# Optimization experiments

Hardware: AMD Instinct MI355X
Metric: run time of the kernel (lower is better)

## Reference

```python
import jax, jax.numpy as jnp
import numpy as np

D_MODEL = 1024
N_HEADS = 16
D_HEAD = D_MODEL // N_HEADS
BATCH = 2
SEQ = 2048


def spectral_linear(x, basis, scales):
    # (x @ U) * s @ U^T ; basis is a fixed (non-learned) square matrix
    return ((x @ basis) * scales) @ basis.T


def setup_inputs() -> dict:
    key = jax.random.key(0)
    ks = jax.random.split(key, 3)
    x = jax.random.normal(ks[0], (BATCH, SEQ, D_MODEL), dtype=jnp.float32)
    # orthonormal-ish spectral basis (random Gaussian scaled keeps values sane)
    basis = jax.random.normal(ks[1], (D_MODEL, D_MODEL), dtype=jnp.float32) / np.sqrt(D_MODEL)
    route_bias = jax.random.normal(ks[2], (N_HEADS, SEQ, SEQ), dtype=jnp.float32) * 0.02
    ones = jnp.ones((D_MODEL,), dtype=jnp.float32)
    return {
        "x": x,
        "basis": basis,
        "scale_q": ones,
        "scale_k": ones,
        "scale_v": ones,
        "scale_o": ones,
        "route_bias": route_bias,
    }


def reference(x, basis, scale_q, scale_k, scale_v, scale_o, route_bias):
    bsz, seq_len, _ = x.shape

    def split_heads(t):  # [b,s,d] -> [b,h,s,dh]
        return t.reshape(bsz, seq_len, N_HEADS, D_HEAD).transpose(0, 2, 1, 3)

    q = split_heads(spectral_linear(x, basis, scale_q))
    k = split_heads(spectral_linear(x, basis, scale_k))
    v = split_heads(spectral_linear(x, basis, scale_v))

    scores = jnp.einsum("bhqd,bhkd->bhqk", q, k) / np.sqrt(D_HEAD).astype(np.float32)
    scores = scores + route_bias[None, :, :seq_len, :seq_len]
    causal = jnp.triu(jnp.ones((seq_len, seq_len), dtype=bool), k=1)
    scores = jnp.where(causal[None, None], -jnp.inf, scores)
    attn = jax.nn.softmax(scores, axis=-1)
    out = jnp.einsum("bhqk,bhkd->bhqd", attn, v)
    out = out.transpose(0, 2, 1, 3).reshape(bsz, seq_len, D_MODEL)
    return spectral_linear(out, basis, scale_o)
```

## Files before the change

kernel.cpp:

```cpp
#include <hip/hip_runtime.h>
#include <stdint.h>

#define AS1 __attribute__((address_space(1)))
#define AS3 __attribute__((address_space(3)))

typedef __bf16 bf16x8 __attribute__((ext_vector_type(8)));
typedef float f32x4 __attribute__((ext_vector_type(4)));

#if defined(__has_builtin)
#if __has_builtin(__builtin_amdgcn_global_load_lds)
#define USE_GLL 1
#else
#define USE_GLL 0
#endif
#else
#define USE_GLL 0
#endif

static __device__ __forceinline__ unsigned short f2bf(float f) {
    union { float f; uint32_t u; } v; v.f = f;
    uint32_t u = v.u + 0x7fffu + ((v.u >> 16) & 1u);
    return (unsigned short)(u >> 16);
}

__global__ void k_prep(const float* __restrict__ x, const float* __restrict__ basis,
                       const float* __restrict__ sq, const float* __restrict__ sk,
                       const float* __restrict__ sv, const float* __restrict__ so,
                       unsigned short* __restrict__ x_bf,
                       unsigned short* __restrict__ Bq, unsigned short* __restrict__ Bk,
                       unsigned short* __restrict__ Bv, unsigned short* __restrict__ Bo,
                       unsigned short* __restrict__ Ub) {
    int b = blockIdx.x;
    if (b < 4096) {
        int idx = b * 256 + threadIdx.x;
        int k = idx & 1023;
        float v = basis[idx];
        Bq[idx] = f2bf(v * sq[k]);
        Bk[idx] = f2bf(v * sk[k]);
        Bv[idx] = f2bf(v * sv[k]);
        Bo[idx] = f2bf(v * so[k]);
        Ub[idx] = f2bf(v);
    } else {
        int idx = ((b - 4096) * 256 + threadIdx.x) * 4;
        float4 v = *(const float4*)(x + idx);
        unsigned short r[4] = { f2bf(v.x), f2bf(v.y), f2bf(v.z), f2bf(v.w) };
        *(uint2*)(x_bf + idx) = *(const uint2*)r;
    }
}

__global__ void k_transpose_v(const unsigned short* __restrict__ vsb, unsigned short* __restrict__ vtb) {
    __shared__ __align__(16) unsigned short t[128 * 72];
    const int sc = blockIdx.x;
    const int bh = blockIdx.y;
    const int tid = threadIdx.x;
    #pragma unroll
    for (int rep = 0; rep < 4; ++rep) {
        int idx = rep * 256 + tid;
        int s = idx >> 3, part = idx & 7;
        *(uint4*)(t + s * 72 + part * 8) =
            *(const uint4*)(vsb + ((size_t)bh * 2048 + sc * 128 + s) * 64 + part * 8);
    }
    __syncthreads();
    #pragma unroll
    for (int rep = 0; rep < 4; ++rep) {
        int idx = rep * 256 + tid;
        int d = idx >> 4, pc = idx & 15;
        unsigned short tmp[8];
        #pragma unroll
        for (int j = 0; j < 8; ++j) tmp[j] = t[(pc * 8 + j) * 72 + d];
        *(uint4*)(vtb + ((size_t)bh * 64 + d) * 2048 + sc * 128 + pc * 8) = *(const uint4*)tmp;
    }
}

__global__ __launch_bounds__(512, 2)
void k_gemm_qkv8(const unsigned short* __restrict__ A,
                 const unsigned short* __restrict__ B,
                 unsigned short* __restrict__ qkv)
{
    __shared__ __align__(16) unsigned short lds[3 * 16384];

    const int tid  = threadIdx.x;
    const int lane = tid & 63;
    const int w    = tid >> 6;
    const int wm   = w & 1;
    const int wn   = w >> 1;
    const int fm   = lane & 15;
    const int quad = lane >> 4;
    const int K    = 1024;
    const int NT   = 32;

    int bid  = blockIdx.y * 12 + blockIdx.x;
    int sbid = (bid & 7) * 24 + (bid >> 3);
    const int bm = sbid / 12;
    const int bn = sbid % 12;

    const int srow = tid >> 2;
    const int sg   = tid & 3;
    const unsigned short* gA = A + ((size_t)(bm * 256) + srow) * K + sg * 8;
    const unsigned short* gB = B + ((size_t)(bn * 256) + srow) * K + sg * 8;

#define STAGE_A8(tt, h) __builtin_amdgcn_global_load_lds( \
        (const void AS1*)(gA + (size_t)(h) * 128 * 1024 + (tt) * 32), \
        (void AS3*)(lds + ((tt) % 3) * 16384 + (h) * 4096 + w * 512), 16, 0, 0)
#define STAGE_B8(tt, h) __builtin_amdgcn_global_load_lds( \
        (const void AS1*)(gB + (size_t)(h) * 128 * 1024 + (tt) * 32), \
        (void AS3*)(lds + ((tt) % 3) * 16384 + 8192 + (h) * 4096 + w * 512), 16, 0, 0)

    f32x4 zero4 = {0.f, 0.f, 0.f, 0.f};
    f32x4 acc[8][4];
    #pragma unroll
    for (int i = 0; i < 8; ++i)
        #pragma unroll
        for (int j = 0; j < 4; ++j) acc[i][j] = zero4;

    STAGE_A8(0, 0); STAGE_A8(0, 1); STAGE_B8(0, 0); STAGE_B8(0, 1);
    STAGE_A8(1, 0); STAGE_A8(1, 1); STAGE_B8(1, 0); STAGE_B8(1, 1);
    asm volatile("s_waitcnt vmcnt(4)" ::: "memory");
    __builtin_amdgcn_s_barrier();

    for (int t = 0; t < NT; ++t) {
        const unsigned short* buf = lds + (t % 3) * 16384;

        bf16x8 bfr[4], af[4];
        #pragma unroll
        for (int j = 0; j < 4; ++j)
            bfr[j] = *(const bf16x8*)(buf + 8192 + (wn * 64 + j * 16 + fm) * 32 + quad * 8);
        #pragma unroll
        for (int i = 0; i < 4; ++i)
            af[i] = *(const bf16x8*)(buf + (wm * 128 + i * 16 + fm) * 32 + quad * 8);
        if (t + 2 < NT) { STAGE_A8(t + 2, 0); STAGE_A8(t + 2, 1); }
        __builtin_amdgcn_s_barrier();
        asm volatile("s_waitcnt lgkmcnt(0)" ::: "memory");
        __builtin_amdgcn_s_setprio(1);
        #pragma unroll
        for (int i = 0; i < 4; ++i)
            #pragma unroll
            for (int j = 0; j < 4; ++j)
                acc[i][j] = __builtin_amdgcn_mfma_f32_16x16x32_bf16(af[i], bfr[j], acc[i][j], 0, 0, 0);
        __builtin_amdgcn_s_setprio(0);
        __builtin_amdgcn_s_barrier();

        bf16x8 af2[4];
        #pragma unroll
        for (int i = 0; i < 4; ++i)
            af2[i] = *(const bf16x8*)(buf + (wm * 128 + 64 + i * 16 + fm) * 32 + quad * 8);
        if (t + 2 < NT) { STAGE_B8(t + 2, 0); STAGE_B8(t + 2, 1); }
        if (t < NT - 2)       asm volatile("s_waitcnt vmcnt(4)" ::: "memory");
        else if (t == NT - 2) asm volatile("s_waitcnt vmcnt(0)" ::: "memory");
        __builtin_amdgcn_s_barrier();
        asm volatile("s_waitcnt lgkmcnt(0)" ::: "memory");
        __builtin_amdgcn_s_setprio(1);
        #pragma unroll
        for (int i = 0; i < 4; ++i)
            #pragma unroll
            for (int j = 0; j < 4; ++j)
                acc[i + 4][j] = __builtin_amdgcn_mfma_f32_16x16x32_bf16(af2[i], bfr[j], acc[i + 4][j], 0, 0, 0);
        __builtin_amdgcn_s_setprio(0);
        __builtin_amdgcn_s_barrier();
    }
#undef STAGE_A8
#undef STAGE_B8

    #pragma unroll
    for (int i = 0; i < 8; ++i)
        #pragma unroll
        for (int j = 0; j < 4; ++j)
            #pragma unroll
            for (int r = 0; r < 4; ++r) {
                int row = bm * 256 + wm * 128 + i * 16 + quad * 4 + r;
                int col = bn * 256 + wn * 64 + j * 16 + fm;
                int sec = col >> 10, cc = col & 1023;
                int bb = row >> 11, s = row & 2047;
                int hh = cc >> 6,  d = cc & 63;
                qkv[((size_t)sec << 22) + (((size_t)(bb * 16 + hh)) * 2048 + s) * 64 + d] = f2bf(acc[i][j][r]);
            }
}

#define BK 32
template<int EPI>
__global__ __launch_bounds__(256, 2)
void k_gemm_n64(const unsigned short* __restrict__ A,
                const unsigned short* __restrict__ B,
                void* __restrict__ Cout,
                int M, int N, int K)
{
    __shared__ __align__(16) unsigned short As[128 * BK];
    __shared__ __align__(16) unsigned short Bs[64 * BK];

    const int tid  = threadIdx.x;
    const int lane = tid & 63;
    const int w    = tid >> 6;
    const int wm   = w & 1;
    const int wn   = w >> 1;
    const int bm   = blockIdx.y;
    const int bn   = blockIdx.x;
    const int fm   = lane & 15;
    const int quad = lane >> 4;
    const int fk   = quad * 8;
    const int srow = lane >> 2;
    const int spart= lane & 3;

    f32x4 zero4 = {0.f, 0.f, 0.f, 0.f};
    f32x4 acc[4][2];
    #pragma unroll
    for (int i = 0; i < 4; ++i)
        #pragma unroll
        for (int j = 0; j < 2; ++j) acc[i][j] = zero4;

    for (int k0 = 0; k0 < K; k0 += BK) {
        #pragma unroll
        for (int t = 0; t < 2; ++t) {
            int row = w * 32 + t * 16 + srow;
            const unsigned short* ga = A + (size_t)(bm * 128 + row) * K + k0 + spart * 8;
#if USE_GLL
            __builtin_amdgcn_global_load_lds((const void AS1*)ga, (void AS3*)(As + w * 1024 + t * 512), 16, 0, 0);
#else
            *(uint4*)(As + w * 1024 + t * 512 + lane * 8) = *(const uint4*)ga;
#endif
        }
        {
            const unsigned short* gb = B + (size_t)(bn * 64 + w * 16 + srow) * K + k0 + spart * 8;
#if USE_GLL
            __builtin_amdgcn_global_load_lds((const void AS1*)gb, (void AS3*)(Bs + w * 512), 16, 0, 0);
#else
            *(uint4*)(Bs + w * 512 + lane * 8) = *(const uint4*)gb;
#endif
        }
        __syncthreads();
        bf16x8 af[4], bfr[2];
        #pragma unroll
        for (int i = 0; i < 4; ++i) af[i] = *(const bf16x8*)(As + (wm * 64 + i * 16 + fm) * BK + fk);
        #pragma unroll
        for (int j = 0; j < 2; ++j) bfr[j] = *(const bf16x8*)(Bs + (wn * 32 + j * 16 + fm) * BK + fk);
        #pragma unroll
        for (int i = 0; i < 4; ++i)
            #pragma unroll
            for (int j = 0; j < 2; ++j)
                acc[i][j] = __builtin_amdgcn_mfma_f32_16x16x32_bf16(af[i], bfr[j], acc[i][j], 0, 0, 0);
        __syncthreads();
    }

    #pragma unroll
    for (int i = 0; i < 4; ++i)
        #pragma unroll
        for (int j = 0; j < 2; ++j)
            #pragma unroll
            for (int r = 0; r < 4; ++r) {
                int row = bm * 128 + wm * 64 + i * 16 + quad * 4 + r;
                int col = bn * 64 + wn * 32 + j * 16 + fm;
                if (EPI == 0) ((unsigned short*)Cout)[(size_t)row * N + col] = f2bf(acc[i][j][r]);
                else          ((float*)Cout)[(size_t)row * N + col] = acc[i][j][r];
            }
}

__global__ __launch_bounds__(256, 2)
void k_attn(const unsigned short* __restrict__ qs, const unsigned short* __restrict__ ks,
            const unsigned short* __restrict__ vt, const float* __restrict__ bias,
            unsigned short* __restrict__ out)
{
    const int qt = 15 - blockIdx.x;
    const int by = blockIdx.y;
    const int h  = by >> 1;
    const int b  = by & 1;
    const int bh = b * 16 + h;
    const size_t rowbase = (size_t)bh * 2048;

    const int tid  = threadIdx.x;
    const int lane = tid & 63;
    const int w    = tid >> 6;
    const int fm   = lane & 15;
    const int quad = lane >> 4;
    const int fk   = quad * 8;

    __shared__ __align__(16) unsigned short Ks[64 * 72];
    __shared__ __align__(16) unsigned short Vt[64 * 72];
    __shared__ __align__(16) unsigned short Ps[4][32 * 72];

    const int q0 = qt * 128 + w * 32;

    bf16x8 qf[2][2];
    #pragma unroll
    for (int g = 0; g < 2; ++g)
        #pragma unroll
        for (int c = 0; c < 2; ++c)
            qf[g][c] = *(const bf16x8*)(qs + (rowbase + q0 + g * 16 + fm) * 64 + c * 32 + fk);

    f32x4 zero4 = {0.f, 0.f, 0.f, 0.f};
    f32x4 oacc[2][4];
    float lsum[2][4];
    #pragma unroll
    for (int g = 0; g < 2; ++g) {
        #pragma unroll
        for (int jd = 0; jd < 4; ++jd) oacc[g][jd] = zero4;
        #pragma unroll
        for (int r = 0; r < 4; ++r) lsum[g][r] = 0.f;
    }

    const int nkt = qt * 2 + 2;
    for (int kt = 0; kt < nkt; ++kt) {
        float bb[2][4][4];
        #pragma unroll
        for (int g = 0; g < 2; ++g)
            #pragma unroll
            for (int jn = 0; jn < 4; ++jn)
                #pragma unroll
                for (int r = 0; r < 4; ++r)
                    bb[g][jn][r] = bias[((size_t)h * 2048 + q0 + g * 16 + quad * 4 + r) * 2048
                                        + kt * 64 + jn * 16 + fm];

        #pragma unroll
        for (int rep = 0; rep < 2; ++rep) {
            int idx  = rep * 256 + tid;
            int row  = idx >> 3;
            int part = idx & 7;
            *(uint4*)(Ks + row * 72 + part * 8) =
                *(const uint4*)(ks + (rowbase + kt * 64 + row) * 64 + part * 8);
            *(uint4*)(Vt + row * 72 + part * 8) =
                *(const uint4*)(vt + ((size_t)bh * 64 + row) * 2048 + kt * 64 + part * 8);
        }
        __syncthreads();

        bf16x8 kb[4][2];
        #pragma unroll
        for (int jn = 0; jn < 4; ++jn)
            #pragma unroll
            for (int c = 0; c < 2; ++c)
                kb[jn][c] = *(const bf16x8*)(Ks + (jn * 16 + fm) * 72 + c * 32 + fk);
        f32x4 sacc[2][4];
        #pragma unroll
        for (int g = 0; g < 2; ++g)
            #pragma unroll
            for (int jn = 0; jn < 4; ++jn) sacc[g][jn] = zero4;
        #pragma unroll
        for (int g = 0; g < 2; ++g)
            #pragma unroll
            for (int jn = 0; jn < 4; ++jn)
                #pragma unroll
                for (int c = 0; c < 2; ++c)
                    sacc[g][jn] = __builtin_amdgcn_mfma_f32_16x16x32_bf16(qf[g][c], kb[jn][c], sacc[g][jn], 0, 0, 0);

        #pragma unroll
        for (int g = 0; g < 2; ++g)
            #pragma unroll
            for (int jn = 0; jn < 4; ++jn)
                #pragma unroll
                for (int r = 0; r < 4; ++r) {
                    int row = q0 + g * 16 + quad * 4 + r;
                    int col = kt * 64 + jn * 16 + fm;
                    float p = exp2f(sacc[g][jn][r] * 0.18033688f + bb[g][jn][r] * 1.44269504f);
                    p = (col > row) ? 0.f : p;
                    lsum[g][r] += p;
                    Ps[w][(g * 16 + quad * 4 + r) * 72 + jn * 16 + fm] = f2bf(p);
                }

        bf16x8 vf[4][2], pf[2][2];
        #pragma unroll
        for (int jd = 0; jd < 4; ++jd)
            #pragma unroll
            for (int c = 0; c < 2; ++c)
                vf[jd][c] = *(const bf16x8*)(Vt + (jd * 16 + fm) * 72 + c * 32 + fk);
        #pragma unroll
        for (int g = 0; g < 2; ++g)
            #pragma unroll
            for (int c = 0; c < 2; ++c)
                pf[g][c] = *(const bf16x8*)(Ps[w] + (g * 16 + fm) * 72 + c * 32 + fk);
        #pragma unroll
        for (int g = 0; g < 2; ++g)
            #pragma unroll
            for (int jd = 0; jd < 4; ++jd)
                #pragma unroll
                for (int c = 0; c < 2; ++c)
                    oacc[g][jd] = __builtin_amdgcn_mfma_f32_16x16x32_bf16(pf[g][c], vf[jd][c], oacc[g][jd], 0, 0, 0);

        __syncthreads();
    }

    #pragma unroll
    for (int g = 0; g < 2; ++g)
        #pragma unroll
        for (int r = 0; r < 4; ++r) {
            float l = lsum[g][r];
            #pragma unroll
            for (int off = 1; off < 16; off <<= 1) l += __shfl_xor(l, off, 64);
            lsum[g][r] = 1.f / l;
        }

    #pragma unroll
    for (int g = 0; g < 2; ++g)
        #pragma unroll
        for (int jd = 0; jd < 4; ++jd)
            #pragma unroll
            for (int r = 0; r < 4; ++r) {
                int row = q0 + g * 16 + quad * 4 + r;
                int d   = jd * 16 + fm;
                out[((size_t)b * 2048 + row) * 1024 + h * 64 + d] = f2bf(oacc[g][jd][r] * lsum[g][r]);
            }
}

extern "C" void kernel_launch(void* const* d_in, const int* in_sizes, int n_in,
                              void* d_out, int out_size, void* d_ws, size_t ws_size,
                              hipStream_t stream) {
    (void)in_sizes; (void)n_in; (void)out_size; (void)ws_size;
    const float* x     = (const float*)d_in[0];
    const float* basis = (const float*)d_in[1];
    const float* sq    = (const float*)d_in[2];
    const float* sk    = (const float*)d_in[3];
    const float* sv    = (const float*)d_in[4];
    const float* so    = (const float*)d_in[5];
    const float* bias  = (const float*)d_in[6];
    float* out = (float*)d_out;

    char* ws = (char*)d_ws;
    size_t off = 0;
    auto alloc = [&](size_t bytes) { void* p = ws + off; off += bytes; return p; };
    unsigned short* x_bf  = (unsigned short*)alloc((size_t)8 << 20);
    unsigned short* Acat  = (unsigned short*)alloc((size_t)8 << 20);
    unsigned short* Ub    = (unsigned short*)alloc((size_t)2 << 20);
    unsigned short* Wall  = (unsigned short*)alloc((size_t)8 << 20);
    unsigned short* qkvb  = (unsigned short*)alloc((size_t)24 << 20);
    unsigned short* vtb   = (unsigned short*)alloc((size_t)8 << 20);
    unsigned short* attno = (unsigned short*)alloc((size_t)8 << 20);

    unsigned short* Bq  = Acat;
    unsigned short* Bk  = Acat + ((size_t)1 << 20);
    unsigned short* Bv  = Acat + ((size_t)2 << 20);
    unsigned short* Bo  = Acat + ((size_t)3 << 20);
    unsigned short* qsb = qkvb;
    unsigned short* ksb = qkvb + ((size_t)1 << 22);
    unsigned short* vsb = qkvb + ((size_t)2 << 22);
    unsigned short* Wo  = Wall + (size_t)3 * 1024 * 1024;

    k_prep<<<8192, 256, 0, stream>>>(x, basis, sq, sk, sv, so, x_bf, Bq, Bk, Bv, Bo, Ub);

    dim3 blk(256);
    k_gemm_n64<0><<<dim3(16, 32), blk, 0, stream>>>(Acat, Ub, Wall, 4096, 1024, 1024);
    k_gemm_qkv8<<<dim3(12, 16), dim3(512), 0, stream>>>(x_bf, Wall, qkvb);
    k_transpose_v<<<dim3(16, 32), blk, 0, stream>>>(vsb, vtb);
    k_attn<<<dim3(16, 32), blk, 0, stream>>>(qsb, ksb, vtb, bias, attno);
    k_gemm_n64<2><<<dim3(16, 32), blk, 0, stream>>>(attno, Wo, out, 4096, 1024, 1024);
}
```

Baseline: 510.5 us.

## Retile QKV GEMM to 256x192 tiles so 256 blocks fill all CUs

The fused QKV GEMM tile width drops from 256 to 192 columns, so the 4096x3072 output splits into 16x16=256 blocks instead of 192. That fills all CUs on the MI355X and reduces wave-quantization tail loss. LDS staging is reshaped with a 3-stage ring for A and part of B, plus extra space for the remaining B rows, and the swizzled block mapping is updated. Launch bounds change to 1 block per CU. Smaller tiles lower per-block arithmetic intensity, and the new B staging layout is more complex.

```diff
diff --git a/kernel.cpp b/kernel.cpp
--- a/kernel.cpp
+++ b/kernel.cpp
@@ -72,12 +72,12 @@
     }
 }
 
-__global__ __launch_bounds__(512, 2)
+__global__ __launch_bounds__(512, 1)
 void k_gemm_qkv8(const unsigned short* __restrict__ A,
                  const unsigned short* __restrict__ B,
                  unsigned short* __restrict__ qkv)
 {
-    __shared__ __align__(16) unsigned short lds[3 * 16384];
+    __shared__ __align__(16) unsigned short lds[45056];
 
     const int tid  = threadIdx.x;
     const int lane = tid & 63;
@@ -89,53 +89,58 @@
     const int K    = 1024;
     const int NT   = 32;
 
-    int bid  = blockIdx.y * 12 + blockIdx.x;
-    int sbid = (bid & 7) * 24 + (bid >> 3);
-    const int bm = sbid / 12;
-    const int bn = sbid % 12;
-
-    const int srow = tid >> 2;
-    const int sg   = tid & 3;
-    const unsigned short* gA = A + ((size_t)(bm * 256) + srow) * K + sg * 8;
-    const unsigned short* gB = B + ((size_t)(bn * 256) + srow) * K + sg * 8;
-
-#define STAGE_A8(tt, h) __builtin_amdgcn_global_load_lds( \
-        (const void AS1*)(gA + (size_t)(h) * 128 * 1024 + (tt) * 32), \
-        (void AS3*)(lds + ((tt) % 3) * 16384 + (h) * 4096 + w * 512), 16, 0, 0)
-#define STAGE_B8(tt, h) __builtin_amdgcn_global_load_lds( \
-        (const void AS1*)(gB + (size_t)(h) * 128 * 1024 + (tt) * 32), \
-        (void AS3*)(lds + ((tt) % 3) * 16384 + 8192 + (h) * 4096 + w * 512), 16, 0, 0)
+    int bid  = blockIdx.y * 16 + blockIdx.x;
+    int sbid = (bid & 7) * 32 + (bid >> 3);
+    const int bm = sbid >> 4;
+    const int bn = sbid & 15;
+
+    const int arow = w * 32 + (lane >> 2);
+    const int brow = ((w < 6) ? w * 32 : (w - 6) * 32) + (lane >> 2);
+    const int sg   = (lane & 3) * 8;
+    const unsigned short* gA = A + ((size_t)(bm * 256) + arow) * K + sg;
+    const unsigned short* gB = B + ((size_t)(bn * 192) + brow) * K + sg;
+
+#define ADST(tt, h) (lds + ((tt) % 3) * 14336 + w * 1024 + (h) * 512)
+#define BDST(tt, h) ((w < 6) ? (lds + ((tt) % 3) * 14336 + 8192 + w * 1024 + (h) * 512) \
+                             : (lds + 43008 + (w - 6) * 1024 + (h) * 512))
+#define STAGE_A(tt, h) __builtin_amdgcn_global_load_lds( \
+        (const void AS1*)(gA + (size_t)(h) * 16 * 1024 + (size_t)(tt) * 32), \
+        (void AS3*)ADST(tt, h), 16, 0, 0)
+#define STAGE_B(tt, h) __builtin_amdgcn_global_load_lds( \
+        (const void AS1*)(gB + (size_t)(h) * 16 * 1024 + (size_t)(tt) * 32), \
+        (void AS3*)BDST(tt, h), 16, 0, 0)
 
     f32x4 zero4 = {0.f, 0.f, 0.f, 0.f};
-    f32x4 acc[8][4];
+    f32x4 acc[8][3];
     #pragma unroll
     for (int i = 0; i < 8; ++i)
         #pragma unroll
-        for (int j = 0; j < 4; ++j) acc[i][j] = zero4;
-
-    STAGE_A8(0, 0); STAGE_A8(0, 1); STAGE_B8(0, 0); STAGE_B8(0, 1);
-    STAGE_A8(1, 0); STAGE_A8(1, 1); STAGE_B8(1, 0); STAGE_B8(1, 1);
+        for (int j = 0; j < 3; ++j) acc[i][j] = zero4;
+
+    STAGE_A(0, 0); STAGE_A(0, 1); STAGE_B(0, 0); STAGE_B(0, 1);
+    STAGE_A(1, 0); STAGE_A(1, 1); STAGE_B(1, 0); STAGE_B(1, 1);
     asm volatile("s_waitcnt vmcnt(4)" ::: "memory");
     __builtin_amdgcn_s_barrier();
 
     for (int t = 0; t < NT; ++t) {
-        const unsigned short* buf = lds + (t % 3) * 16384;
-
-        bf16x8 bfr[4], af[4];
-        #pragma unroll
-        for (int j = 0; j < 4; ++j)
-            bfr[j] = *(const bf16x8*)(buf + 8192 + (wn * 64 + j * 16 + fm) * 32 + quad * 8);
+        const unsigned short* buf  = lds + (t % 3) * 14336;
+        const unsigned short* bufB = buf + 8192;
+
+        bf16x8 bfr[3], af[4];
+        #pragma unroll
+        for (int j = 0; j < 3; ++j)
+            bfr[j] = *(const bf16x8*)(bufB + (wn * 48 + j * 16 + fm) * 32 + quad * 8);
         #pragma unroll
         for (int i = 0; i < 4; ++i)
             af[i] = *(const bf16x8*)(buf + (wm * 128 + i * 16 + fm) * 32 + quad * 8);
-        if (t + 2 < NT) { STAGE_A8(t + 2, 0); STAGE_A8(t + 2, 1); }
+        if (t + 2 < NT) { STAGE_A(t + 2, 0); STAGE_A(t + 2, 1); }
         __builtin_amdgcn_s_barrier();
         asm volatile("s_waitcnt lgkmcnt(0)" ::: "memory");
         __builtin_amdgcn_s_setprio(1);
         #pragma unroll
         for (int i = 0; i < 4; ++i)
             #pragma unroll
-            for (int j = 0; j < 4; ++j)
+            for (int j = 0; j < 3; ++j)
                 acc[i][j] = __builtin_amdgcn_mfma_f32_16x16x32_bf16(af[i], bfr[j], acc[i][j], 0, 0, 0);
         __builtin_amdgcn_s_setprio(0);
         __builtin_amdgcn_s_barrier();
@@ -144,7 +149,7 @@
         #pragma unroll
         for (int i = 0; i < 4; ++i)
             af2[i] = *(const bf16x8*)(buf + (wm * 128 + 64 + i * 16 + fm) * 32 + quad * 8);
-        if (t + 2 < NT) { STAGE_B8(t + 2, 0); STAGE_B8(t + 2, 1); }
+        if (t + 2 < NT) { STAGE_B(t + 2, 0); STAGE_B(t + 2, 1); }
         if (t < NT - 2)       asm volatile("s_waitcnt vmcnt(4)" ::: "memory");
         else if (t == NT - 2) asm volatile("s_waitcnt vmcnt(0)" ::: "memory");
         __builtin_amdgcn_s_barrier();
@@ -153,22 +158,24 @@
         #pragma unroll
         for (int i = 0; i < 4; ++i)
             #pragma unroll
-            for (int j = 0; j < 4; ++j)
+            for (int j = 0; j < 3; ++j)
                 acc[i + 4][j] = __builtin_amdgcn_mfma_f32_16x16x32_bf16(af2[i], bfr[j], acc[i + 4][j], 0, 0, 0);
         __builtin_amdgcn_s_setprio(0);
         __builtin_amdgcn_s_barrier();
     }
-#undef STAGE_A8
-#undef STAGE_B8
+#undef STAGE_A
+#undef STAGE_B
+#undef ADST
+#undef BDST
 
     #pragma unroll
     for (int i = 0; i < 8; ++i)
         #pragma unroll
-        for (int j = 0; j < 4; ++j)
+        for (int j = 0; j < 3; ++j)
             #pragma unroll
             for (int r = 0; r < 4; ++r) {
                 int row = bm * 256 + wm * 128 + i * 16 + quad * 4 + r;
-                int col = bn * 256 + wn * 64 + j * 16 + fm;
+                int col = bn * 192 + wn * 48 + j * 16 + fm;
                 int sec = col >> 10, cc = col & 1023;
                 int bb = row >> 11, s = row & 2047;
                 int hh = cc >> 6,  d = cc & 63;
@@ -434,7 +441,7 @@
 
     dim3 blk(256);
     k_gemm_n64<0><<<dim3(16, 32), blk, 0, stream>>>(Acat, Ub, Wall, 4096, 1024, 1024);
-    k_gemm_qkv8<<<dim3(12, 16), dim3(512), 0, stream>>>(x_bf, Wall, qkvb);
+    k_gemm_qkv8<<<dim3(16, 16), dim3(512), 0, stream>>>(x_bf, Wall, qkvb);
     k_transpose_v<<<dim3(16, 32), blk, 0, stream>>>(vsb, vtb);
     k_attn<<<dim3(16, 32), blk, 0, stream>>>(qsb, ksb, vtb, bias, attno);
     k_gemm_n64<2><<<dim3(16, 32), blk, 0, stream>>>(attno, Wo, out, 4096, 1024, 1024);
```

Result: no change. 507.0 us (-0.7%).
